# Performance work log

Hardware: AMD Instinct MI355X
Metric: run time of the kernel (lower is better)

Reference implementation:

```python
import jax, jax.numpy as jnp
import numpy as np

ROPE_BASE = 10000.0

def rope_tables(n, r):
    inv = 1.0 / (ROPE_BASE ** (jnp.arange(0, r, 2, dtype=jnp.float32) / r))  # [r/2]
    ang = jnp.arange(n, dtype=jnp.float32)[:, None] * inv[None, :]           # [n, r/2]
    cos = jnp.concatenate([jnp.cos(ang), jnp.cos(ang)], axis=-1)             # [n, r]
    sin = jnp.concatenate([jnp.sin(ang), jnp.sin(ang)], axis=-1)
    return cos, sin

def apply_rope(x, cos, sin):
    # x: [B, H, T, r]; cos/sin: [T, r]
    half = x.shape[-1] // 2
    x_rot = jnp.concatenate([-x[..., half:], x[..., :half]], axis=-1)
    return x * cos + x_rot * sin

def setup_inputs() -> dict:
    key = jax.random.key(0)
    ks = jax.random.split(key, 8)
    B, S, L = 2, 1024, 1024
    dim_q, h, k, d_c, d_cq, r = 2048, 16, 128, 512, 1536, 64
    w = 0.02  # weight scale to keep activations numerically tame
    return {
        'hidden_q': jax.random.normal(ks[0], (B, S, dim_q), jnp.float32),
        'kv_c':     jax.random.normal(ks[1], (B, L, d_c), jnp.float32),
        'Wq':       jax.random.normal(ks[2], (h * k, dim_q), jnp.float32) * w,
        'w_kc_q':   jax.random.normal(ks[3], (h, k, d_cq), jnp.float32) * w,
        'W_qr':     jax.random.normal(ks[4], (h, d_cq, r), jnp.float32) * (w / np.sqrt(r)),
        'W_kr':     jax.random.normal(ks[5], (h, d_c, r), jnp.float32) * w,
        'w_kc_kv':  jax.random.normal(ks[6], (h, k, d_c), jnp.float32) * w,
        'Wo':       jax.random.normal(ks[7], (dim_q, h * k), jnp.float32) * w,
    }

def reference(hidden_q, kv_c, Wq, w_kc_q, W_qr, W_kr, w_kc_kv, Wo):
    B, S, _ = hidden_q.shape
    L = kv_c.shape[1]
    h, k, _ = w_kc_q.shape
    r = W_qr.shape[-1]
    # q projection: [B,S,h,k]
    q_hk = (hidden_q @ Wq.T).reshape(B, S, h, k)
    # low-rank expand to q-compressed space then retrieval space
    q_big = jnp.einsum('bshk,hkq->bshq', q_hk, w_kc_q)          # [B,S,h,d_cq]
    q_r = jnp.einsum('bshq,hqr->bhsr', q_big, W_qr)             # [B,h,S,r]
    k_r = jnp.einsum('bld,hdr->bhlr', kv_c, W_kr)               # [B,h,L,r]
    cos_S, sin_S = rope_tables(S, r)
    cos_L, sin_L = rope_tables(L, r)
    q_r = apply_rope(q_r, cos_S, sin_S)
    k_r = apply_rope(k_r, cos_L, sin_L)
    # attention in retrieval space, values are compressed kv (shared across heads)
    scores = jnp.einsum('bhsr,bhlr->bhsl', q_r, k_r)            # scale baked into W_qr
    attn = jax.nn.softmax(scores, axis=-1)
    ctx_c = jnp.einsum('bhsl,bld->bhsd', attn, kv_c)            # [B,h,S,d_c]
    # decompress per head: w_kc_kv is [h,k,d_c]
    ctx_lat = jnp.einsum('bhsd,hkd->bshk', ctx_c, w_kc_kv).reshape(B, S, h * k)
    return ctx_lat @ Wo.T
```

## Files before the change

kernel.cpp:

```cpp
#include <hip/hip_runtime.h>
#include <math.h>
#include <stdint.h>


typedef __attribute__((ext_vector_type(8))) short short8;
typedef __attribute__((ext_vector_type(4))) float f32x4;

#define GLOAD16(gsrc, ldst)                                                            \
  __builtin_amdgcn_global_load_lds((const __attribute__((address_space(1))) void*)(gsrc), \
                                   (__attribute__((address_space(3))) void*)(ldst), 16, 0, 0)

__device__ inline uint16_t f2b(float x) {
  uint32_t u = __builtin_bit_cast(uint32_t, x);
  u += 0x7fff + ((u >> 16) & 1);
  return (uint16_t)(u >> 16);
}
__device__ inline float b2f(uint16_t b) {
  uint32_t u = ((uint32_t)b) << 16;
  return __builtin_bit_cast(float, u);
}
__device__ inline uint32_t cvtpk_bf16(float lo, float hi) {
  uint32_t d;
  asm("v_cvt_pk_bf16_f32 %0, %1, %2" : "=v"(d) : "v"(lo), "v"(hi));
  return d;
}

__global__ __launch_bounds__(256) void prep_kernel(
    const float* __restrict__ s0, uint16_t* __restrict__ t0, const float* __restrict__ s1,
    uint16_t* __restrict__ t1, const float* __restrict__ s2, uint16_t* __restrict__ t2,
    const float* __restrict__ s3, uint16_t* __restrict__ t3, const float* __restrict__ s4,
    uint16_t* __restrict__ t4, float* __restrict__ cosK, float* __restrict__ sinK,
    float* __restrict__ cosQ, float* __restrict__ sinQ, const float* __restrict__ Wq,
    uint16_t* __restrict__ WqT, const float* __restrict__ W_qr, uint16_t* __restrict__ WqrT,
    const float* __restrict__ W_kr, uint16_t* __restrict__ WkrT) {
  __shared__ float t[32][33];
  int bid = blockIdx.x;
  if (bid >= 6912) {
    int tb = bid - 6912;
    const float* src;
    uint16_t* dst;
    int R, C, r0, c0;
    if (tb < 4096) {
      src = Wq; dst = WqT; R = 2048; C = 2048;
      r0 = (tb & 63) * 32; c0 = (tb >> 6) * 32;
    } else if (tb < 5632) {
      int b = tb - 4096;
      int z = b / 96, rem = b % 96;
      src = W_qr + (size_t)z * 98304; dst = WqrT + (size_t)z * 98304;
      R = 1536; C = 64;
      r0 = (rem >> 1) * 32; c0 = (rem & 1) * 32;
    } else {
      int b = tb - 5632;
      int z = b / 32, rem = b % 32;
      src = W_kr + (size_t)z * 32768; dst = WkrT + (size_t)z * 32768;
      R = 512; C = 64;
      r0 = (rem >> 1) * 32; c0 = (rem & 1) * 32;
    }
    int tr = threadIdx.x >> 5, tc = threadIdx.x & 31;
#pragma unroll
    for (int i = 0; i < 4; ++i) t[tr + i * 8][tc] = src[(size_t)(r0 + tr + i * 8) * C + c0 + tc];
    __syncthreads();
#pragma unroll
    for (int i = 0; i < 4; ++i)
      dst[(size_t)(c0 + tr + i * 8) * R + r0 + tc] = f2b(t[tc][tr + i * 8]);
    return;
  }
  if (bid >= 6656) {
    const float LOG2E = 1.44269504088896341f;
    int idx = (bid - 6656) * 256 + threadIdx.x;
    int s = idx >> 6, j = idx & 63;
    int i = j & 31;
    float inv = powf(10000.0f, -(float)(2 * i) / 64.0f);
    float ang = (float)s * inv;
    float c = cosf(ang), sn = sinf(ang);
    cosK[idx] = c;
    sinK[idx] = sn;
    cosQ[idx] = c * LOG2E;
    sinQ[idx] = sn * LOG2E;
    return;
  }
  const float* s;
  uint16_t* tt;
  int off;
  if (bid < 2048) { s = s0; tt = t0; off = bid; }
  else if (bid < 2560) { s = s1; tt = t1; off = bid - 2048; }
  else if (bid < 3072) { s = s2; tt = t2; off = bid - 2560; }
  else if (bid < 5120) { s = s3; tt = t3; off = bid - 3072; }
  else { s = s4; tt = t4; off = bid - 5120; }
  int i = off * 256 + threadIdx.x;
  const float4* s4v = (const float4*)s;
  float4 a = s4v[i * 2], b = s4v[i * 2 + 1];
  union {
    uint16_t u[8];
    uint4 v;
  } o;
  o.u[0] = f2b(a.x); o.u[1] = f2b(a.y); o.u[2] = f2b(a.z); o.u[3] = f2b(a.w);
  o.u[4] = f2b(b.x); o.u[5] = f2b(b.y); o.u[6] = f2b(b.z); o.u[7] = f2b(b.w);
  ((uint4*)tt)[i] = o.v;
}

template <int BM, int EPI, int SPLITK = 1>
__global__ __launch_bounds__(256) void gemm_mfma_kernel(
    const uint16_t* __restrict__ A, const uint16_t* __restrict__ Bt, void* __restrict__ Cv, int K,
    int lda, int ldb, int ldc, int aZ, int bZ, int cZ, const float* __restrict__ rc,
    const float* __restrict__ rs, const uint16_t* __restrict__ Bt2, void* __restrict__ Cv2) {
  constexpr int MT = BM / 32;
  __shared__ __align__(16) uint16_t As[2][BM * 64];
  __shared__ __align__(16) uint16_t Bs[2][128 * 64];
  int z = blockIdx.z;
  if (SPLITK > 1) {
    int zh = z / SPLITK, zk = z % SPLITK;
    A += (size_t)zh * aZ + (size_t)zk * K;
    Bt += (size_t)zh * bZ + (size_t)zk * K;
  } else {
    A += (size_t)z * aZ;
    Bt += (size_t)z * bZ;
  }
  int n0;
  if (EPI == 4) {
    if (blockIdx.y >= 8) {
      Bt = Bt2;
      n0 = (blockIdx.y - 8) * 128;
    } else {
      n0 = blockIdx.y * 128;
    }
  } else {
    n0 = blockIdx.y * 128;
  }
  int m0 = blockIdx.x * BM;
  int tid = threadIdx.x;
  int wave = tid >> 6, lane = tid & 63;
  int wm = wave >> 1, wn = wave & 1;
  int rS = lane >> 3, sl = lane & 7;
  int lr = lane >> 4, lc = lane & 15;

  auto stage = [&](int k0, int buf) {
#pragma unroll
    for (int i = 0; i < MT; ++i) {
      int idx = wave * MT + i;
      int row = idx * 8 + rS;
      GLOAD16(A + (size_t)(m0 + row) * lda + k0 + ((sl ^ (row & 7)) << 3),
              (uint8_t*)As[buf] + idx * 1024);
    }
#pragma unroll
    for (int i = 0; i < 4; ++i) {
      int idx = wave * 4 + i;
      int row = idx * 8 + rS;
      GLOAD16(Bt + (size_t)(n0 + row) * ldb + k0 + ((sl ^ (row & 7)) << 3),
              (uint8_t*)Bs[buf] + idx * 1024);
    }
  };

  f32x4 acc[MT][4] = {};
  stage(0, 0);
  int cur = 0;
  for (int k0 = 0; k0 < K; k0 += 64) {
    __syncthreads();
    if (k0 + 64 < K) stage(k0 + 64, cur ^ 1);
    short8 af[MT][2], bf[4][2];
#pragma unroll
    for (int t = 0; t < MT; ++t)
#pragma unroll
      for (int ks = 0; ks < 2; ++ks) {
        int slot = ks * 4 + lr;
        int ra = wm * (BM / 2) + t * 16 + lc;
        af[t][ks] =
            *(const short8*)((const uint8_t*)As[cur] + ra * 128 + ((slot ^ (ra & 7)) << 4));
      }
#pragma unroll
    for (int t = 0; t < 4; ++t)
#pragma unroll
      for (int ks = 0; ks < 2; ++ks) {
        int slot = ks * 4 + lr;
        int rb = wn * 64 + t * 16 + lc;
        bf[t][ks] =
            *(const short8*)((const uint8_t*)Bs[cur] + rb * 128 + ((slot ^ (rb & 7)) << 4));
      }
    __builtin_amdgcn_s_setprio(1);
#pragma unroll
    for (int mt = 0; mt < MT; ++mt)
#pragma unroll
      for (int nt = 0; nt < 4; ++nt) {
        acc[mt][nt] =
            __builtin_amdgcn_mfma_f32_16x16x32_bf16(af[mt][0], bf[nt][0], acc[mt][nt], 0, 0, 0);
        acc[mt][nt] =
            __builtin_amdgcn_mfma_f32_16x16x32_bf16(af[mt][1], bf[nt][1], acc[mt][nt], 0, 0, 0);
      }
    __builtin_amdgcn_s_setprio(0);
    cur ^= 1;
  }
  bool ropePath = (EPI == 3) || (EPI == 4 && blockIdx.y < 8);
  if (ropePath) {
#pragma unroll
    for (int mt = 0; mt < MT; ++mt)
#pragma unroll
      for (int nt = 0; nt < 4; ++nt)
#pragma unroll
        for (int r = 0; r < 4; ++r) {
          int m = m0 + wm * (BM / 2) + mt * 16 + lr * 4 + r;
          int n = n0 + wn * 64 + nt * 16 + lc;
          int pos = m & 1023, j = n & 63;
          float x = acc[mt][nt][r];
          float prt = acc[mt][nt ^ 2][r];
          float rot = (nt & 2) ? prt : -prt;
          float v = fmaf(x, rc[pos * 64 + j], rot * rs[pos * 64 + j]);
          ((uint16_t*)Cv)[(size_t)m * ldc + n] = f2b(v);
        }
  } else if (EPI == 4 || EPI == 2) {
    void* Cd = (EPI == 4) ? Cv2 : Cv;
#pragma unroll
    for (int mt = 0; mt < MT; ++mt)
#pragma unroll
      for (int nt = 0; nt < 4; ++nt)
#pragma unroll
        for (int r = 0; r < 4; ++r) {
          int m = m0 + wm * (BM / 2) + mt * 16 + lr * 4 + r;
          int n = n0 + wn * 64 + nt * 16 + lc;
          ((uint16_t*)Cd)[((size_t)((m >> 10) * 2048 + n)) * 1024 + (m & 1023)] =
              f2b(acc[mt][nt][r]);
        }
  } else {
#pragma unroll
    for (int mt = 0; mt < MT; ++mt)
#pragma unroll
      for (int nt = 0; nt < 4; ++nt)
#pragma unroll
        for (int r = 0; r < 4; ++r) {
          int m = m0 + wm * (BM / 2) + mt * 16 + lr * 4 + r;
          int n = n0 + wn * 64 + nt * 16 + lc;
          float v = acc[mt][nt][r];
          if (EPI == 0)
            ((float*)Cv)[(size_t)z * cZ + (size_t)m * ldc + n] = v;
          else
            ((uint16_t*)Cv)[(size_t)z * cZ + (size_t)m * ldc + n] = f2b(v);
        }
  }
}

__global__ __launch_bounds__(256) void reduce1_kernel(const float* __restrict__ tp,
                                                      uint16_t* __restrict__ tmpT) {
  int gid = blockIdx.x * 256 + threadIdx.x;
  int zh = gid >> 13, e = gid & 8191;
  const float* b = tp + (size_t)zh * 32768 + e;
  tmpT[gid] = f2b(b[0] + b[8192] + b[16384] + b[24576]);
}

__global__ __launch_bounds__(512, 2) void flash3_kernel(const uint16_t* __restrict__ qrb,
                                                        const uint16_t* __restrict__ krb,
                                                        const uint16_t* __restrict__ VhT,
                                                        uint16_t* __restrict__ ctxlatb) {
  __shared__ __align__(16) uint8_t lds[67584];
  int bh = blockIdx.x;
  int b = bh >> 4, h = bh & 15;
  int s0 = blockIdx.y * 128;
  int tid = threadIdx.x, wave = tid >> 6, lane = tid & 63;
  int lr = lane >> 4, lc = lane & 15;
  int rS = lane >> 3, sl = lane & 7;

  uint8_t* Ps = lds + 49152 + wave * 2304;

  const uint16_t* qrow = qrb + (size_t)(b * 1024 + s0 + wave * 16 + lc) * 1024 + h * 64;
  short8 qa[2];
  qa[0] = *(const short8*)(qrow + lr * 8);
  qa[1] = *(const short8*)(qrow + 32 + lr * 8);

  float l_run = 0.f;
  f32x4 o[8] = {};

  uint8_t* psW = Ps + lc * 144 + lr * 8;
  const uint8_t* psR = Ps + lc * 144 + lr * 16;

  const uint16_t* krbase = krb + (size_t)(b * 1024) * 1024 + h * 64;
  const uint16_t* vtbase = VhT + (size_t)(b * 2048 + h * 128) * 1024;

  auto stageKV = [&](int l0, int buf) {
#pragma unroll
    for (int i = 0; i < 3; ++i) {
      int g = wave * 3 + i;
      if (g < 8) {
        int row = g * 8 + rS;
        GLOAD16(krbase + (size_t)(l0 + row) * 1024 + ((sl ^ (row & 7)) << 3),
                lds + buf * 8192 + g * 1024);
      } else {
        int v = g - 8;
        int row = v * 8 + rS;
        GLOAD16(vtbase + (size_t)row * 1024 + l0 + ((sl ^ (row & 7)) << 3),
                lds + 16384 + buf * 16384 + v * 1024);
      }
    }
  };

  stageKV(0, 0);
  int cur = 0;
  for (int t = 0; t < 16; ++t) {
    __syncthreads();
    if (t < 15) stageKV((t + 1) * 64, cur ^ 1);
    const uint8_t* Ks = lds + cur * 8192;
    const uint8_t* Vs = lds + 16384 + cur * 16384;

    f32x4 sc[4];
    __builtin_amdgcn_s_setprio(1);
#pragma unroll
    for (int nt = 0; nt < 4; ++nt) {
      int rowk = nt * 16 + lc;
      short8 kb0 = *(const short8*)(Ks + rowk * 128 + ((lr ^ (rowk & 7)) << 4));
      short8 kb1 = *(const short8*)(Ks + rowk * 128 + (((4 + lr) ^ (rowk & 7)) << 4));
      f32x4 z = {};
      z = __builtin_amdgcn_mfma_f32_16x16x32_bf16(kb0, qa[0], z, 0, 0, 0);
      sc[nt] = __builtin_amdgcn_mfma_f32_16x16x32_bf16(kb1, qa[1], z, 0, 0, 0);
    }
    __builtin_amdgcn_s_setprio(0);

    float ps = 0.f;
#pragma unroll
    for (int nt = 0; nt < 4; ++nt) {
#pragma unroll
      for (int rp = 0; rp < 2; ++rp) {
        float p0 = exp2f(sc[nt][rp * 2] - 8.0f);
        float p1 = exp2f(sc[nt][rp * 2 + 1] - 8.0f);
        ps += p0 + p1;
        *(uint32_t*)(psW + nt * 32 + rp * 4) = cvtpk_bf16(p0, p1);
      }
    }
    l_run += ps;

    short8 pa[2];
    pa[0] = *(const short8*)(psR);
    pa[1] = *(const short8*)(psR + 64);
    __builtin_amdgcn_s_setprio(1);
#pragma unroll
    for (int nt = 0; nt < 8; ++nt) {
      int rowv = nt * 16 + lc;
      short8 vb0 = *(const short8*)(Vs + rowv * 128 + ((lr ^ (rowv & 7)) << 4));
      short8 vb1 = *(const short8*)(Vs + rowv * 128 + (((4 + lr) ^ (rowv & 7)) << 4));
      o[nt] = __builtin_amdgcn_mfma_f32_16x16x32_bf16(pa[0], vb0, o[nt], 0, 0, 0);
      o[nt] = __builtin_amdgcn_mfma_f32_16x16x32_bf16(pa[1], vb1, o[nt], 0, 0, 0);
    }
    __builtin_amdgcn_s_setprio(0);
    cur ^= 1;
  }

  l_run += __shfl_xor(l_run, 16);
  l_run += __shfl_xor(l_run, 32);
  float li[4];
#pragma unroll
  for (int r = 0; r < 4; ++r) li[r] = 1.0f / __shfl(l_run, lr * 4 + r);
  uint16_t* orow = ctxlatb + (size_t)(b * 1024 + s0 + wave * 16) * 2048 + h * 128;
#pragma unroll
  for (int nt = 0; nt < 8; ++nt)
#pragma unroll
    for (int r = 0; r < 4; ++r)
      orow[(size_t)(lr * 4 + r) * 2048 + nt * 16 + lc] = f2b(o[nt][r] * li[r]);
}

extern "C" void kernel_launch(void* const* d_in, const int* in_sizes, int n_in,
                              void* d_out, int out_size, void* d_ws, size_t ws_size,
                              hipStream_t stream) {
  const float* hidden_q = (const float*)d_in[0];
  const float* kv_c = (const float*)d_in[1];
  const float* Wq = (const float*)d_in[2];
  const float* w_kc_q = (const float*)d_in[3];
  const float* W_qr = (const float*)d_in[4];
  const float* W_kr = (const float*)d_in[5];
  const float* w_kc_kv = (const float*)d_in[6];
  const float* Wo = (const float*)d_in[7];
  float* out = (float*)d_out;

  const size_t MB = 1024 * 1024;
  uint8_t* base = (uint8_t*)d_ws;
  uint16_t* Wob = (uint16_t*)(base + 0 * MB);
  uint16_t* qrb = (uint16_t*)(base + 8 * MB);
  uint16_t* krb = (uint16_t*)(base + 12 * MB);
  uint16_t* VhT = (uint16_t*)(base + 16 * MB);
  uint16_t* ctxlatb = (uint16_t*)(base + 24 * MB);
  float* cosK = (float*)(base + 32 * MB);
  float* sinK = (float*)(base + 32 * MB + 262144);
  float* cosQ = (float*)(base + 32 * MB + 524288);
  float* sinQ = (float*)(base + 32 * MB + 786432);
  uint16_t* hqb = (uint16_t*)(base + 33 * MB);
  uint16_t* kvb = (uint16_t*)(base + 41 * MB);
  uint16_t* wkvb = (uint16_t*)(base + 43 * MB);
  uint16_t* WqT = (uint16_t*)(base + 45 * MB);
  uint16_t* WqrT = (uint16_t*)(base + 53 * MB);
  uint16_t* wkcqb = (uint16_t*)(base + 56 * MB);
  float* tmp1 = (float*)(base + 62 * MB);
  uint16_t* tmpT = (uint16_t*)(base + 64 * MB);
  uint16_t* WkrT = (uint16_t*)(base + 64 * MB + 262144);

  prep_kernel<<<dim3(13056), dim3(256), 0, stream>>>(
      hidden_q, hqb, kv_c, kvb, w_kc_kv, wkvb, Wo, Wob, w_kc_q, wkcqb, cosK, sinK, cosQ, sinQ, Wq,
      WqT, (const float*)W_qr, WqrT, (const float*)W_kr, WkrT);
  gemm_mfma_kernel<64, 0, 4><<<dim3(1, 1, 64), dim3(256), 0, stream>>>(
      WqrT, wkcqb, tmp1, 384, 1536, 1536, 128, 98304, 196608, 8192, nullptr, nullptr, nullptr,
      nullptr);
  reduce1_kernel<<<dim3(512), dim3(256), 0, stream>>>(tmp1, tmpT);
  uint16_t* WfoldT = wkcqb;
  gemm_mfma_kernel<64, 1><<<dim3(1, 16, 16), dim3(256), 0, stream>>>(
      tmpT, WqT, WfoldT, 128, 128, 2048, 2048, 8192, 128, 131072, nullptr, nullptr, nullptr,
      nullptr);
  gemm_mfma_kernel<64, 3><<<dim3(32, 8), dim3(256), 0, stream>>>(
      hqb, WfoldT, qrb, 2048, 2048, 2048, 1024, 0, 0, 0, cosQ, sinQ, nullptr, nullptr);
  gemm_mfma_kernel<64, 4><<<dim3(32, 24), dim3(256), 0, stream>>>(
      kvb, WkrT, krb, 512, 512, 512, 1024, 0, 0, 0, cosK, sinK, wkvb, VhT);
  flash3_kernel<<<dim3(32, 8), dim3(512), 0, stream>>>(qrb, krb, VhT, ctxlatb);
  gemm_mfma_kernel<64, 0><<<dim3(32, 16), dim3(256), 0, stream>>>(
      ctxlatb, Wob, out, 2048, 2048, 2048, 2048, 0, 0, 0, nullptr, nullptr, nullptr, nullptr);
}
```

Before: 135.3 us.

## Fuse split-K reduction into fold GEMM and merge three projection GEMMs into one launch

The separate split-K reduce kernel is removed. The new fold2 kernel sums the four fp32 partials, converts them to bf16 and writes them straight into swizzled LDS as its A operand. The q-rope, k-rope and V projection GEMMs are merged into a single 32x32-grid launch that picks its operands and epilogue by blockIdx.y. This cuts two kernel launches and one global round trip. It also lets the short K=512 blocks run alongside the long K=2048 ones, at the cost of uneven per-block work inside one grid.

Result: faster. 129.0 us (-4.7%).

```diff
diff --git a/kernel.cpp b/kernel.cpp
--- a/kernel.cpp
+++ b/kernel.cpp
@@ -100,10 +100,11 @@
 }
 
 template <int BM, int EPI, int SPLITK = 1>
-__global__ __launch_bounds__(256) void gemm_mfma_kernel(
-    const uint16_t* __restrict__ A, const uint16_t* __restrict__ Bt, void* __restrict__ Cv, int K,
-    int lda, int ldb, int ldc, int aZ, int bZ, int cZ, const float* __restrict__ rc,
-    const float* __restrict__ rs, const uint16_t* __restrict__ Bt2, void* __restrict__ Cv2) {
+__global__ __launch_bounds__(256) void gemm_mfma_kernel(const uint16_t* __restrict__ A,
+                                                        const uint16_t* __restrict__ Bt,
+                                                        void* __restrict__ Cv, int K, int lda,
+                                                        int ldb, int ldc, int aZ, int bZ,
+                                                        int cZ) {
   constexpr int MT = BM / 32;
   __shared__ __align__(16) uint16_t As[2][BM * 64];
   __shared__ __align__(16) uint16_t Bs[2][128 * 64];
@@ -116,18 +117,7 @@
     A += (size_t)z * aZ;
     Bt += (size_t)z * bZ;
   }
-  int n0;
-  if (EPI == 4) {
-    if (blockIdx.y >= 8) {
-      Bt = Bt2;
-      n0 = (blockIdx.y - 8) * 128;
-    } else {
-      n0 = blockIdx.y * 128;
-    }
-  } else {
-    n0 = blockIdx.y * 128;
-  }
-  int m0 = blockIdx.x * BM;
+  int m0 = blockIdx.x * BM, n0 = blockIdx.y * 128;
   int tid = threadIdx.x;
   int wave = tid >> 6, lane = tid & 63;
   int wm = wave >> 1, wn = wave & 1;
@@ -189,60 +179,235 @@
     __builtin_amdgcn_s_setprio(0);
     cur ^= 1;
   }
-  bool ropePath = (EPI == 3) || (EPI == 4 && blockIdx.y < 8);
-  if (ropePath) {
-#pragma unroll
-    for (int mt = 0; mt < MT; ++mt)
+#pragma unroll
+  for (int mt = 0; mt < MT; ++mt)
+#pragma unroll
+    for (int nt = 0; nt < 4; ++nt)
+#pragma unroll
+      for (int r = 0; r < 4; ++r) {
+        int m = m0 + wm * (BM / 2) + mt * 16 + lr * 4 + r;
+        int n = n0 + wn * 64 + nt * 16 + lc;
+        float v = acc[mt][nt][r];
+        if (EPI == 0)
+          ((float*)Cv)[(size_t)z * cZ + (size_t)m * ldc + n] = v;
+        else
+          ((uint16_t*)Cv)[(size_t)z * cZ + (size_t)m * ldc + n] = f2b(v);
+      }
+}
+
+__global__ __launch_bounds__(256) void fold2_kernel(const float* __restrict__ tmp1,
+                                                    const uint16_t* __restrict__ WqT,
+                                                    uint16_t* __restrict__ WfoldT) {
+  __shared__ __align__(16) uint16_t As[2][64 * 64];
+  __shared__ __align__(16) uint16_t Bs[2][128 * 64];
+  int z = blockIdx.z;
+  int n0 = blockIdx.y * 128;
+  const uint16_t* Bt = WqT + z * 128;
+  int tid = threadIdx.x;
+  int wave = tid >> 6, lane = tid & 63;
+  int wm = wave >> 1, wn = wave & 1;
+  int rS = lane >> 3, sl = lane & 7;
+  int lr = lane >> 4, lc = lane & 15;
+
+  {
+    int row = tid >> 2;
+    int kbase = (tid & 3) * 32;
+    const float* tp = tmp1 + (size_t)z * 32768 + row * 128;
+#pragma unroll
+    for (int c = 0; c < 8; ++c) {
+      int k4 = kbase + c * 4;
+      float4 s = *(const float4*)(tp + k4);
+      float4 s1 = *(const float4*)(tp + 8192 + k4);
+      float4 s2 = *(const float4*)(tp + 16384 + k4);
+      float4 s3 = *(const float4*)(tp + 24576 + k4);
+      s.x = ((s.x + s1.x) + s2.x) + s3.x;
+      s.y = ((s.y + s1.y) + s2.y) + s3.y;
+      s.z = ((s.z + s1.z) + s2.z) + s3.z;
+      s.w = ((s.w + s1.w) + s2.w) + s3.w;
+      uint32_t lo = cvtpk_bf16(s.x, s.y);
+      uint32_t hi = cvtpk_bf16(s.z, s.w);
+      int buf = k4 >> 6, kl = k4 & 63;
+      int slot = kl >> 3;
+      uint32_t addr = row * 128 + ((slot ^ (row & 7)) << 4) + (kl & 7) * 2;
+      *(uint32_t*)((uint8_t*)As[buf] + addr) = lo;
+      *(uint32_t*)((uint8_t*)As[buf] + addr + 4) = hi;
+    }
+  }
+
+  auto stageB = [&](int k0, int buf) {
+#pragma unroll
+    for (int i = 0; i < 4; ++i) {
+      int idx = wave * 4 + i;
+      int row = idx * 8 + rS;
+      GLOAD16(Bt + (size_t)(n0 + row) * 2048 + k0 + ((sl ^ (row & 7)) << 3),
+              (uint8_t*)Bs[buf] + idx * 1024);
+    }
+  };
+
+  f32x4 acc[2][4] = {};
+  stageB(0, 0);
+  int cur = 0;
+  for (int k0 = 0; k0 < 128; k0 += 64) {
+    __syncthreads();
+    if (k0 + 64 < 128) stageB(64, 1);
+    short8 af[2][2], bf[4][2];
+#pragma unroll
+    for (int t = 0; t < 2; ++t)
+#pragma unroll
+      for (int ks = 0; ks < 2; ++ks) {
+        int slot = ks * 4 + lr;
+        int ra = wm * 32 + t * 16 + lc;
+        af[t][ks] =
+            *(const short8*)((const uint8_t*)As[cur] + ra * 128 + ((slot ^ (ra & 7)) << 4));
+      }
+#pragma unroll
+    for (int t = 0; t < 4; ++t)
+#pragma unroll
+      for (int ks = 0; ks < 2; ++ks) {
+        int slot = ks * 4 + lr;
+        int rb = wn * 64 + t * 16 + lc;
+        bf[t][ks] =
+            *(const short8*)((const uint8_t*)Bs[cur] + rb * 128 + ((slot ^ (rb & 7)) << 4));
+      }
+    __builtin_amdgcn_s_setprio(1);
+#pragma unroll
+    for (int mt = 0; mt < 2; ++mt)
+#pragma unroll
+      for (int nt = 0; nt < 4; ++nt) {
+        acc[mt][nt] =
+            __builtin_amdgcn_mfma_f32_16x16x32_bf16(af[mt][0], bf[nt][0], acc[mt][nt], 0, 0, 0);
+        acc[mt][nt] =
+            __builtin_amdgcn_mfma_f32_16x16x32_bf16(af[mt][1], bf[nt][1], acc[mt][nt], 0, 0, 0);
+      }
+    __builtin_amdgcn_s_setprio(0);
+    cur ^= 1;
+  }
+#pragma unroll
+  for (int mt = 0; mt < 2; ++mt)
+#pragma unroll
+    for (int nt = 0; nt < 4; ++nt)
+#pragma unroll
+      for (int r = 0; r < 4; ++r) {
+        int m = wm * 32 + mt * 16 + lr * 4 + r;
+        int n = n0 + wn * 64 + nt * 16 + lc;
+        WfoldT[(size_t)z * 131072 + (size_t)m * 2048 + n] = f2b(acc[mt][nt][r]);
+      }
+}
+
+__global__ __launch_bounds__(256) void gemm_triple_kernel(
+    const uint16_t* __restrict__ hqb, const uint16_t* __restrict__ WfoldT,
+    uint16_t* __restrict__ qrb, const uint16_t* __restrict__ kvb,
+    const uint16_t* __restrict__ WkrT, uint16_t* __restrict__ krb,
+    const uint16_t* __restrict__ wkvb, uint16_t* __restrict__ VhT,
+    const float* __restrict__ cosQ, const float* __restrict__ sinQ,
+    const float* __restrict__ cosK, const float* __restrict__ sinK) {
+  __shared__ __align__(16) uint16_t As[2][64 * 64];
+  __shared__ __align__(16) uint16_t Bs[2][128 * 64];
+  int bx = blockIdx.x, byr = blockIdx.y;
+  const uint16_t *A, *Bt;
+  uint16_t* Cv;
+  const float *rc, *rs;
+  int K, lda, ldb, n0, mode;
+  if (byr < 8) {
+    A = hqb; Bt = WfoldT; Cv = qrb; K = 2048; lda = 2048; ldb = 2048;
+    n0 = byr * 128; mode = 0; rc = cosQ; rs = sinQ;
+  } else if (byr < 16) {
+    A = kvb; Bt = WkrT; Cv = krb; K = 512; lda = 512; ldb = 512;
+    n0 = (byr - 8) * 128; mode = 0; rc = cosK; rs = sinK;
+  } else {
+    A = kvb; Bt = wkvb; Cv = VhT; K = 512; lda = 512; ldb = 512;
+    n0 = (byr - 16) * 128; mode = 1; rc = nullptr; rs = nullptr;
+  }
+  int m0 = bx * 64;
+  int tid = threadIdx.x;
+  int wave = tid >> 6, lane = tid & 63;
+  int wm = wave >> 1, wn = wave & 1;
+  int rS = lane >> 3, sl = lane & 7;
+  int lr = lane >> 4, lc = lane & 15;
+
+  auto stage = [&](int k0, int buf) {
+#pragma unroll
+    for (int i = 0; i < 2; ++i) {
+      int idx = wave * 2 + i;
+      int row = idx * 8 + rS;
+      GLOAD16(A + (size_t)(m0 + row) * lda + k0 + ((sl ^ (row & 7)) << 3),
+              (uint8_t*)As[buf] + idx * 1024);
+    }
+#pragma unroll
+    for (int i = 0; i < 4; ++i) {
+      int idx = wave * 4 + i;
+      int row = idx * 8 + rS;
+      GLOAD16(Bt + (size_t)(n0 + row) * ldb + k0 + ((sl ^ (row & 7)) << 3),
+              (uint8_t*)Bs[buf] + idx * 1024);
+    }
+  };
+
+  f32x4 acc[2][4] = {};
+  stage(0, 0);
+  int cur = 0;
+  for (int k0 = 0; k0 < K; k0 += 64) {
+    __syncthreads();
+    if (k0 + 64 < K) stage(k0 + 64, cur ^ 1);
+    short8 af[2][2], bf[4][2];
+#pragma unroll
+    for (int t = 0; t < 2; ++t)
+#pragma unroll
+      for (int ks = 0; ks < 2; ++ks) {
+        int slot = ks * 4 + lr;
+        int ra = wm * 32 + t * 16 + lc;
+        af[t][ks] =
+            *(const short8*)((const uint8_t*)As[cur] + ra * 128 + ((slot ^ (ra & 7)) << 4));
+      }
+#pragma unroll
+    for (int t = 0; t < 4; ++t)
+#pragma unroll
+      for (int ks = 0; ks < 2; ++ks) {
+        int slot = ks * 4 + lr;
+        int rb = wn * 64 + t * 16 + lc;
+        bf[t][ks] =
+            *(const short8*)((const uint8_t*)Bs[cur] + rb * 128 + ((slot ^ (rb & 7)) << 4));
+      }
+    __builtin_amdgcn_s_setprio(1);
+#pragma unroll
+    for (int mt = 0; mt < 2; ++mt)
+#pragma unroll
+      for (int nt = 0; nt < 4; ++nt) {
+        acc[mt][nt] =
+            __builtin_amdgcn_mfma_f32_16x16x32_bf16(af[mt][0], bf[nt][0], acc[mt][nt], 0, 0, 0);
+        acc[mt][nt] =
+            __builtin_amdgcn_mfma_f32_16x16x32_bf16(af[mt][1], bf[nt][1], acc[mt][nt], 0, 0, 0);
+      }
+    __builtin_amdgcn_s_setprio(0);
+    cur ^= 1;
+  }
+  if (mode == 0) {
+#pragma unroll
+    for (int mt = 0; mt < 2; ++mt)
 #pragma unroll
       for (int nt = 0; nt < 4; ++nt)
 #pragma unroll
         for (int r = 0; r < 4; ++r) {
-          int m = m0 + wm * (BM / 2) + mt * 16 + lr * 4 + r;
+          int m = m0 + wm * 32 + mt * 16 + lr * 4 + r;
           int n = n0 + wn * 64 + nt * 16 + lc;
           int pos = m & 1023, j = n & 63;
           float x = acc[mt][nt][r];
           float prt = acc[mt][nt ^ 2][r];
           float rot = (nt & 2) ? prt : -prt;
           float v = fmaf(x, rc[pos * 64 + j], rot * rs[pos * 64 + j]);
-          ((uint16_t*)Cv)[(size_t)m * ldc + n] = f2b(v);
-        }
-  } else if (EPI == 4 || EPI == 2) {
-    void* Cd = (EPI == 4) ? Cv2 : Cv;
-#pragma unroll
-    for (int mt = 0; mt < MT; ++mt)
-#pragma unroll
-      for (int nt = 0; nt < 4; ++nt)
-#pragma unroll
-        for (int r = 0; r < 4; ++r) {
-          int m = m0 + wm * (BM / 2) + mt * 16 + lr * 4 + r;
-          int n = n0 + wn * 64 + nt * 16 + lc;
-          ((uint16_t*)Cd)[((size_t)((m >> 10) * 2048 + n)) * 1024 + (m & 1023)] =
-              f2b(acc[mt][nt][r]);
+          Cv[(size_t)m * 1024 + n] = f2b(v);
         }
   } else {
 #pragma unroll
-    for (int mt = 0; mt < MT; ++mt)
+    for (int mt = 0; mt < 2; ++mt)
 #pragma unroll
       for (int nt = 0; nt < 4; ++nt)
 #pragma unroll
         for (int r = 0; r < 4; ++r) {
-          int m = m0 + wm * (BM / 2) + mt * 16 + lr * 4 + r;
+          int m = m0 + wm * 32 + mt * 16 + lr * 4 + r;
           int n = n0 + wn * 64 + nt * 16 + lc;
-          float v = acc[mt][nt][r];
-          if (EPI == 0)
-            ((float*)Cv)[(size_t)z * cZ + (size_t)m * ldc + n] = v;
-          else
-            ((uint16_t*)Cv)[(size_t)z * cZ + (size_t)m * ldc + n] = f2b(v);
+          Cv[((size_t)((m >> 10) * 2048 + n)) * 1024 + (m & 1023)] = f2b(acc[mt][nt][r]);
         }
   }
-}
-
-__global__ __launch_bounds__(256) void reduce1_kernel(const float* __restrict__ tp,
-                                                      uint16_t* __restrict__ tmpT) {
-  int gid = blockIdx.x * 256 + threadIdx.x;
-  int zh = gid >> 13, e = gid & 8191;
-  const float* b = tp + (size_t)zh * 32768 + e;
-  tmpT[gid] = f2b(b[0] + b[8192] + b[16384] + b[24576]);
 }
 
 __global__ __launch_bounds__(512, 2) void flash3_kernel(const uint16_t* __restrict__ qrb,
@@ -384,25 +549,18 @@
   uint16_t* WqrT = (uint16_t*)(base + 53 * MB);
   uint16_t* wkcqb = (uint16_t*)(base + 56 * MB);
   float* tmp1 = (float*)(base + 62 * MB);
-  uint16_t* tmpT = (uint16_t*)(base + 64 * MB);
   uint16_t* WkrT = (uint16_t*)(base + 64 * MB + 262144);
 
   prep_kernel<<<dim3(13056), dim3(256), 0, stream>>>(
       hidden_q, hqb, kv_c, kvb, w_kc_kv, wkvb, Wo, Wob, w_kc_q, wkcqb, cosK, sinK, cosQ, sinQ, Wq,
       WqT, (const float*)W_qr, WqrT, (const float*)W_kr, WkrT);
   gemm_mfma_kernel<64, 0, 4><<<dim3(1, 1, 64), dim3(256), 0, stream>>>(
-      WqrT, wkcqb, tmp1, 384, 1536, 1536, 128, 98304, 196608, 8192, nullptr, nullptr, nullptr,
-      nullptr);
-  reduce1_kernel<<<dim3(512), dim3(256), 0, stream>>>(tmp1, tmpT);
+      WqrT, wkcqb, tmp1, 384, 1536, 1536, 128, 98304, 196608, 8192);
   uint16_t* WfoldT = wkcqb;
-  gemm_mfma_kernel<64, 1><<<dim3(1, 16, 16), dim3(256), 0, stream>>>(
-      tmpT, WqT, WfoldT, 128, 128, 2048, 2048, 8192, 128, 131072, nullptr, nullptr, nullptr,
-      nullptr);
-  gemm_mfma_kernel<64, 3><<<dim3(32, 8), dim3(256), 0, stream>>>(
-      hqb, WfoldT, qrb, 2048, 2048, 2048, 1024, 0, 0, 0, cosQ, sinQ, nullptr, nullptr);
-  gemm_mfma_kernel<64, 4><<<dim3(32, 24), dim3(256), 0, stream>>>(
-      kvb, WkrT, krb, 512, 512, 512, 1024, 0, 0, 0, cosK, sinK, wkvb, VhT);
+  fold2_kernel<<<dim3(1, 16, 16), dim3(256), 0, stream>>>(tmp1, WqT, WfoldT);
+  gemm_triple_kernel<<<dim3(32, 32), dim3(256), 0, stream>>>(
+      hqb, WfoldT, qrb, kvb, WkrT, krb, wkvb, VhT, cosQ, sinQ, cosK, sinK);
   flash3_kernel<<<dim3(32, 8), dim3(512), 0, stream>>>(qrb, krb, VhT, ctxlatb);
-  gemm_mfma_kernel<64, 0><<<dim3(32, 16), dim3(256), 0, stream>>>(
-      ctxlatb, Wob, out, 2048, 2048, 2048, 2048, 0, 0, 0, nullptr, nullptr, nullptr, nullptr);
-}
+  gemm_mfma_kernel<64, 0><<<dim3(32, 16), dim3(256), 0, stream>>>(ctxlatb, Wob, out, 2048, 2048,
+                                                                  2048, 2048, 0, 0, 0);
+}
```
